# Kernel optimization log

Measured on AMD Instinct MI355X. Metric: run time of the kernel, lower is better.

## Reference

```python
import jax, jax.numpy as jnp
import numpy as np

_EPSILON = 1e-06
EPS = 0.05
MAX_ITER = 50
THRESHOLD = 0.001


def setup_inputs() -> dict:
    key = jax.random.key(0)
    k1, k2 = jax.random.split(key)
    source = jax.random.normal(k1, (8192, 64), dtype=jnp.float32)
    target = jax.random.normal(k2, (8192, 64), dtype=jnp.float32)
    return {"source": source, "target": target}


def _sinkhorn(source, target):
    source = source.astype(jnp.float32)
    target = target.astype(jnp.float32)
    # squared euclidean cost matrix [N, M] (cdist(p=2)**2)
    sq_s = jnp.sum(source * source, axis=1, keepdims=True)          # [N,1]
    sq_t = jnp.sum(target * target, axis=1, keepdims=True).T        # [1,M]
    cost = sq_s + sq_t - 2.0 * (source @ target.T)                  # [N,M]
    cost = jnp.maximum(cost, 0.0)

    n_source, n_target = cost.shape
    log_mu = jnp.full((n_source,), jnp.log(jnp.maximum(1.0 / n_source, _EPSILON)), dtype=jnp.float32)
    log_nu = jnp.full((n_target,), jnp.log(jnp.maximum(1.0 / n_target, _EPSILON)), dtype=jnp.float32)

    u0 = jnp.zeros((n_source,), dtype=jnp.float32)
    v0 = jnp.zeros((n_target,), dtype=jnp.float32)

    def step(carry, _):
        u, v, done = carry
        prev_u = u
        mc = (-cost + u[:, None] + v[None, :]) / EPS
        u_new = EPS * (log_mu - jax.nn.logsumexp(mc, axis=1)) + u
        mc2 = (-cost + u_new[:, None] + v[None, :]) / EPS
        v_new = EPS * (log_nu - jax.nn.logsumexp(mc2, axis=0)) + v
        # freeze state once converged (emulates the torch early break)
        u = jnp.where(done, u, u_new)
        v = jnp.where(done, v, v_new)
        done = done | (jnp.mean(jnp.abs(u_new - prev_u)) < THRESHOLD)
        return (u, v, done), None

    (u, v, _), _ = jax.lax.scan(step, (u0, v0, jnp.array(False)), None, length=MAX_ITER)

    transport_plan = jnp.exp((-cost + u[:, None] + v[None, :]) / EPS)
    return jnp.sum(transport_plan * cost)


def reference(source, target):
    return _sinkhorn(source, target)
```

## Files before the change

kernel.cpp:

```cpp
#include <hip/hip_runtime.h>

#define N      8192
#define KDIM   64
#define SCALE2     28.853900817779268f
#define INV_SCALE2 0.034657359027997264f
#define TWOSCALE   57.707801635558536f
#define EPSLN2     0.034657359027997264f
#define EPS_LOG_MU (-0.45054566736396444f)
#define THRESH     0.001f
#define NEG_BIG    (-1e30f)
#define NCHUNK  32
#define COLSPAN 256
#define NCT     16
#define ROWS_PER_BLOCK 128

typedef __attribute__((ext_vector_type(8))) short bf16x8;
typedef __attribute__((ext_vector_type(4))) float f32x4;

static __device__ __forceinline__ float exp2fast(float x) { return __builtin_amdgcn_exp2f(x); }
static __device__ __forceinline__ float log2fast(float x) { return __builtin_amdgcn_logf(x); }

static __device__ __forceinline__ unsigned short f2bf(float f) {
    unsigned u = __float_as_uint(f);
    u += 0x7FFFu + ((u >> 16) & 1u);
    return (unsigned short)(u >> 16);
}
static __device__ __forceinline__ float bf2f(unsigned short h) {
    return __uint_as_float(((unsigned)h) << 16);
}

static __device__ __forceinline__ void load16_to_lds(const void* gptr, void* lptr) {
    __builtin_amdgcn_global_load_lds(
        (const __attribute__((address_space(1))) unsigned int*)gptr,
        (__attribute__((address_space(3))) unsigned int*)lptr,
        16, 0, 0);
}

static __device__ __forceinline__ void stage_tile(
        const unsigned short* __restrict__ CPhi, const unsigned short* __restrict__ CPlo,
        char* ldsbuf, int jb, int wave, int swz) {
    const char* gsrc = (const char*)(wave < 2 ? CPhi : CPlo);
    const char* g = gsrc + (size_t)jb * 128 + (size_t)((wave & 1) * 1024 + swz);
    char* l = ldsbuf + (wave & 1) * 1024 + (wave >> 1) * 2048;
    load16_to_lds(g, l);
}

static __device__ __forceinline__ void load_held(
        const unsigned short* __restrict__ RPhi, const unsigned short* __restrict__ RPlo,
        int rowbase, int lrow, int kgrp, bf16x8 (&bh)[2][2], bf16x8 (&bl)[2][2]) {
#pragma unroll
    for (int it = 0; it < 2; ++it)
#pragma unroll
        for (int ks = 0; ks < 2; ++ks) {
            int boff = (rowbase + it * 16 + lrow) * KDIM + ks * 32 + kgrp * 8;
            bh[it][ks] = *reinterpret_cast<const bf16x8*>(RPhi + boff);
            bl[it][ks] = *reinterpret_cast<const bf16x8*>(RPlo + boff);
            asm volatile("" : "+v"(bh[it][ks]));
            asm volatile("" : "+v"(bl[it][ks]));
        }
}

static __device__ __forceinline__ void lse_loop(
        const unsigned short* __restrict__ CPhi, const unsigned short* __restrict__ CPlo,
        char* ldsA, const float* lds_alpha,
        const bf16x8 (&bh)[2][2], const bf16x8 (&bl)[2][2],
        int jbase0, int wave, int lane, int swz, float (&m)[2], float (&s)[2]) {
    const int lrow = lane & 15, kgrp = lane >> 4;
    const int ro = lrow * 128;
    const int x0 = ((kgrp)     ^ (lrow & 7)) * 16;
    const int x1 = ((kgrp + 4) ^ (lrow & 7)) * 16;
    int jb = jbase0;
    int buf = 0;
    for (int ct = 0; ct < NCT; ++ct) {
        if (ct + 1 < NCT)
            stage_tile(CPhi, CPlo, ldsA + ((buf ^ 1) << 12), jb + 16, wave, swz);

        float4 av = *reinterpret_cast<const float4*>(lds_alpha + ct * 16 + kgrp * 4);
        const char* base = ldsA + (buf << 12);
        bf16x8 ah0 = *reinterpret_cast<const bf16x8*>(base + ro + x0);
        bf16x8 ah1 = *reinterpret_cast<const bf16x8*>(base + ro + x1);
        bf16x8 al0 = *reinterpret_cast<const bf16x8*>(base + 2048 + ro + x0);
        bf16x8 al1 = *reinterpret_cast<const bf16x8*>(base + 2048 + ro + x1);

        f32x4 acc0 = {0.0f, 0.0f, 0.0f, 0.0f};
        f32x4 acc1 = {0.0f, 0.0f, 0.0f, 0.0f};
        acc0 = __builtin_amdgcn_mfma_f32_16x16x32_bf16(ah0, bh[0][0], acc0, 0, 0, 0);
        acc1 = __builtin_amdgcn_mfma_f32_16x16x32_bf16(ah0, bh[1][0], acc1, 0, 0, 0);
        acc0 = __builtin_amdgcn_mfma_f32_16x16x32_bf16(ah1, bh[0][1], acc0, 0, 0, 0);
        acc1 = __builtin_amdgcn_mfma_f32_16x16x32_bf16(ah1, bh[1][1], acc1, 0, 0, 0);
        acc0 = __builtin_amdgcn_mfma_f32_16x16x32_bf16(al0, bh[0][0], acc0, 0, 0, 0);
        acc1 = __builtin_amdgcn_mfma_f32_16x16x32_bf16(al0, bh[1][0], acc1, 0, 0, 0);
        acc0 = __builtin_amdgcn_mfma_f32_16x16x32_bf16(al1, bh[0][1], acc0, 0, 0, 0);
        acc1 = __builtin_amdgcn_mfma_f32_16x16x32_bf16(al1, bh[1][1], acc1, 0, 0, 0);
        acc0 = __builtin_amdgcn_mfma_f32_16x16x32_bf16(ah0, bl[0][0], acc0, 0, 0, 0);
        acc1 = __builtin_amdgcn_mfma_f32_16x16x32_bf16(ah0, bl[1][0], acc1, 0, 0, 0);
        acc0 = __builtin_amdgcn_mfma_f32_16x16x32_bf16(ah1, bl[0][1], acc0, 0, 0, 0);
        acc1 = __builtin_amdgcn_mfma_f32_16x16x32_bf16(ah1, bl[1][1], acc1, 0, 0, 0);

#pragma unroll
        for (int it = 0; it < 2; ++it) {
            f32x4 a = (it == 0) ? acc0 : acc1;
            float L0 = fmaf(TWOSCALE, a[0], av.x);
            float L1 = fmaf(TWOSCALE, a[1], av.y);
            float L2 = fmaf(TWOSCALE, a[2], av.z);
            float L3 = fmaf(TWOSCALE, a[3], av.w);
            float mx = fmaxf(fmaxf(L0, L1), fmaxf(L2, L3));
            float mn = fmaxf(m[it], mx);
            float rs = exp2fast(m[it] - mn);
            float e  = (exp2fast(L0 - mn) + exp2fast(L1 - mn)) +
                       (exp2fast(L2 - mn) + exp2fast(L3 - mn));
            s[it] = fmaf(s[it], rs, e);
            m[it] = mn;
        }
        __syncthreads();
        buf ^= 1; jb += 16;
    }
}

static __device__ __forceinline__ void write_partials(
        float (&m)[2], float (&s)[2], float* __restrict__ pm, float* __restrict__ ps,
        const float* __restrict__ sqr2, int ck, int rowbase, int lane) {
    const int lrow = lane & 15, kgrp = lane >> 4;
#pragma unroll
    for (int off = 16; off < 64; off <<= 1) {
#pragma unroll
        for (int it = 0; it < 2; ++it) {
            float mo = __shfl_xor(m[it], off);
            float so = __shfl_xor(s[it], off);
            float mn = fmaxf(m[it], mo);
            s[it] = s[it] * exp2fast(m[it] - mn) + so * exp2fast(mo - mn);
            m[it] = mn;
        }
    }
    if (kgrp == 0) {
#pragma unroll
        for (int it = 0; it < 2; ++it) {
            int row = rowbase + it * 16 + lrow;
            pm[(size_t)ck * N + row] = m[it] - sqr2[row];
            ps[(size_t)ck * N + row] = s[it];
        }
    }
}

__global__ void norms_kernel(const float* __restrict__ S, const float* __restrict__ T,
                             float* __restrict__ sq_s2, float* __restrict__ sq_t2) {
    int t = blockIdx.x * blockDim.x + threadIdx.x;
    const float* p = (t < N) ? S : T;
    int r = t & (N - 1);
    const float4* row = reinterpret_cast<const float4*>(p + (size_t)r * KDIM);
    float acc = 0.0f;
#pragma unroll
    for (int q = 0; q < KDIM / 4; ++q) {
        float4 a = row[q];
        acc += a.x * a.x + a.y * a.y + a.z * a.z + a.w * a.w;
    }
    if (t < N) sq_s2[r] = acc * SCALE2; else sq_t2[r] = acc * SCALE2;
}

__global__ void init_kernel(float* u, float* v, float* alphaT,
                            const float* __restrict__ sq_t2, int* doneArr) {
    int t = blockIdx.x * blockDim.x + threadIdx.x;
    if (t < N) { u[t] = 0.0f; v[t] = 0.0f; alphaT[t] = -sq_t2[t]; }
    if (t == 0) { doneArr[0] = 0; doneArr[1] = 0; }
}

__global__ void split_kernel(const float* __restrict__ S, const float* __restrict__ T,
                             unsigned short* __restrict__ Shi, unsigned short* __restrict__ Slo,
                             unsigned short* __restrict__ Thi, unsigned short* __restrict__ Tlo) {
    int t = blockIdx.x * 256 + threadIdx.x;
    const int half = (N * KDIM) / 4;
    const float* src = (t < half) ? S : T;
    unsigned short* dhi = (t < half) ? Shi : Thi;
    unsigned short* dlo = (t < half) ? Slo : Tlo;
    int e = (t < half) ? t : t - half;
    float4 x = reinterpret_cast<const float4*>(src)[e];
    unsigned short h0 = f2bf(x.x), h1 = f2bf(x.y), h2 = f2bf(x.z), h3 = f2bf(x.w);
    ushort4 hv = make_ushort4(h0, h1, h2, h3);
    ushort4 lv = make_ushort4(f2bf(x.x - bf2f(h0)), f2bf(x.y - bf2f(h1)),
                              f2bf(x.z - bf2f(h2)), f2bf(x.w - bf2f(h3)));
    reinterpret_cast<ushort4*>(dhi)[e] = hv;
    reinterpret_cast<ushort4*>(dlo)[e] = lv;
}

__global__ __launch_bounds__(256, 6) void row_lse(
        const unsigned short* __restrict__ CPhi, const unsigned short* __restrict__ CPlo,
        const unsigned short* __restrict__ RPhi, const unsigned short* __restrict__ RPlo,
        const float* __restrict__ alphaG, const float* __restrict__ sqr2,
        float* __restrict__ pm, float* __restrict__ ps,
        const int* __restrict__ done) {
    if (*done) return;
    __shared__ __align__(16) char ldsA[2 * 4096];
    __shared__ __align__(16) float lds_alpha[COLSPAN];
    const int wave = threadIdx.x >> 6, lane = threadIdx.x & 63;
    const int lrow = lane & 15, kgrp = lane >> 4;
    const int ck = blockIdx.x & 31, rb = blockIdx.x >> 5;
    const int rowbase = rb * ROWS_PER_BLOCK + wave * 32;
    const int jbase0 = ck * COLSPAN;
    const int swz = (lane >> 3) * 128 + (((lane & 7) ^ ((lane >> 3) & 7)) << 4);

    stage_tile(CPhi, CPlo, ldsA, jbase0, wave, swz);
    lds_alpha[threadIdx.x] = alphaG[jbase0 + threadIdx.x];

    bf16x8 bh[2][2], bl[2][2];
    load_held(RPhi, RPlo, rowbase, lrow, kgrp, bh, bl);

    float m[2] = {NEG_BIG, NEG_BIG}, s[2] = {0.0f, 0.0f};
    __syncthreads();

    lse_loop(CPhi, CPlo, ldsA, lds_alpha, bh, bl, jbase0, wave, lane, swz, m, s);
    write_partials(m, s, pm, ps, sqr2, ck, rowbase, lane);
}

__global__ __launch_bounds__(256, 6) void col_lse(
        const unsigned short* __restrict__ CPhi, const unsigned short* __restrict__ CPlo,
        const unsigned short* __restrict__ RPhi, const unsigned short* __restrict__ RPlo,
        const float* __restrict__ pm_in, const float* __restrict__ ps_in,
        const float* __restrict__ sqs2,
        float* __restrict__ u,
        float* __restrict__ blockDiff,
        const float* __restrict__ sqr2,
        float* __restrict__ pm, float* __restrict__ ps,
        const int* __restrict__ done) {
    if (*done) return;
    __shared__ __align__(16) char ldsA[2 * 4096];
    __shared__ __align__(16) float lds_alpha[COLSPAN];
    __shared__ float wsum[4];
    const int wave = threadIdx.x >> 6, lane = threadIdx.x & 63;
    const int lrow = lane & 15, kgrp = lane >> 4;
    const int ck = blockIdx.x & 31, rb = blockIdx.x >> 5;
    const int rowbase = rb * ROWS_PER_BLOCK + wave * 32;
    const int jbase0 = ck * COLSPAN;
    const int swz = (lane >> 3) * 128 + (((lane & 7) ^ ((lane >> 3) & 7)) << 4);

    stage_tile(CPhi, CPlo, ldsA, jbase0, wave, swz);

    {
        int j = jbase0 + threadIdx.x;
        float mm = NEG_BIG, ss = 0.0f;
#pragma unroll
        for (int c = 0; c < NCHUNK; ++c) {
            float mc = pm_in[(size_t)c * N + j];
            float sc = ps_in[(size_t)c * N + j];
            float mn = fmaxf(mm, mc);
            ss = ss * exp2fast(mm - mn) + sc * exp2fast(mc - mn);
            mm = mn;
        }
        float unew = EPS_LOG_MU - EPSLN2 * (mm + log2fast(ss));
        lds_alpha[threadIdx.x] = fmaf(unew, SCALE2, -sqs2[j]);
        if (rb == 0) {
            float d = fabsf(unew - u[j]);
            u[j] = unew;
#pragma unroll
            for (int off = 32; off; off >>= 1) d += __shfl_xor(d, off);
            if (lane == 0) wsum[wave] = d;
        }
    }

    bf16x8 bh[2][2], bl[2][2];
    load_held(RPhi, RPlo, rowbase, lrow, kgrp, bh, bl);

    float m[2] = {NEG_BIG, NEG_BIG}, s[2] = {0.0f, 0.0f};
    __syncthreads();
    if (rb == 0 && threadIdx.x == 0)
        blockDiff[ck] = wsum[0] + wsum[1] + wsum[2] + wsum[3];

    lse_loop(CPhi, CPlo, ldsA, lds_alpha, bh, bl, jbase0, wave, lane, swz, m, s);
    write_partials(m, s, pm, ps, sqr2, ck, rowbase, lane);
}

__global__ __launch_bounds__(256) void v_reduce(const float* __restrict__ pm,
                                                const float* __restrict__ ps,
                                                float* __restrict__ v,
                                                float* __restrict__ alphaT,
                                                const float* __restrict__ sqt2,
                                                const float* __restrict__ blockDiff,
                                                const int* __restrict__ dcur,
                                                int* __restrict__ dnext) {
    if (*dcur) {
        if (blockIdx.x == 0 && threadIdx.x == 0) *dnext = 1;
        return;
    }
    int j = blockIdx.x * 256 + threadIdx.x;
    float m = NEG_BIG, s = 0.0f;
#pragma unroll
    for (int c = 0; c < NCHUNK; ++c) {
        float mc = pm[(size_t)c * N + j];
        float sc = ps[(size_t)c * N + j];
        float mn = fmaxf(m, mc);
        s = s * exp2fast(m - mn) + sc * exp2fast(mc - mn);
        m = mn;
    }
    float vnew = EPS_LOG_MU - EPSLN2 * (m + log2fast(s));
    v[j] = vnew;
    alphaT[j] = fmaf(vnew, SCALE2, -sqt2[j]);

    if (blockIdx.x == 0 && threadIdx.x < 64) {
        float sum = (threadIdx.x < 32) ? blockDiff[threadIdx.x] : 0.0f;
#pragma unroll
        for (int off = 32; off; off >>= 1) sum += __shfl_xor(sum, off);
        if (threadIdx.x == 0)
            *dnext = (sum * (1.0f / (float)N) < THRESH) ? 1 : 0;
    }
}

__global__ __launch_bounds__(256, 6) void plan_mfma(
        const unsigned short* __restrict__ CPhi, const unsigned short* __restrict__ CPlo,
        const unsigned short* __restrict__ RPhi, const unsigned short* __restrict__ RPlo,
        const float* __restrict__ u, const float* __restrict__ v,
        const float* __restrict__ sqr2, const float* __restrict__ sqc2,
        float* __restrict__ part) {
    __shared__ __align__(16) char ldsA[2 * 4096];
    __shared__ __align__(16) float lds_v2[COLSPAN];
    __shared__ __align__(16) float lds_sqc[COLSPAN];
    __shared__ float wsum[4];
    const int wave = threadIdx.x >> 6, lane = threadIdx.x & 63;
    const int lrow = lane & 15, kgrp = lane >> 4;
    const int ck = blockIdx.x & 31, rb = blockIdx.x >> 5;
    const int rowbase = rb * ROWS_PER_BLOCK + wave * 32;
    const int jbase0 = ck * COLSPAN;
    const int swz = (lane >> 3) * 128 + (((lane & 7) ^ ((lane >> 3) & 7)) << 4);

    stage_tile(CPhi, CPlo, ldsA, jbase0, wave, swz);
    lds_v2[threadIdx.x]  = v[jbase0 + threadIdx.x] * SCALE2;
    lds_sqc[threadIdx.x] = sqc2[jbase0 + threadIdx.x];

    bf16x8 bh[2][2], bl[2][2];
    load_held(RPhi, RPlo, rowbase, lrow, kgrp, bh, bl);

    float sqr_i[2], u2_i[2];
#pragma unroll
    for (int it = 0; it < 2; ++it) {
        int row = rowbase + it * 16 + lrow;
        sqr_i[it] = sqr2[row];
        u2_i[it]  = u[row] * SCALE2;
    }

    float lsum = 0.0f;
    __syncthreads();

    const int ro = lrow * 128;
    const int x0 = ((kgrp)     ^ (lrow & 7)) * 16;
    const int x1 = ((kgrp + 4) ^ (lrow & 7)) * 16;
    int jb = jbase0;
    int buf = 0;
    for (int ct = 0; ct < NCT; ++ct) {
        if (ct + 1 < NCT)
            stage_tile(CPhi, CPlo, ldsA + ((buf ^ 1) << 12), jb + 16, wave, swz);

        float4 v2 = *reinterpret_cast<const float4*>(lds_v2 + ct * 16 + kgrp * 4);
        float4 sc = *reinterpret_cast<const float4*>(lds_sqc + ct * 16 + kgrp * 4);
        const char* base = ldsA + (buf << 12);
        bf16x8 ah0 = *reinterpret_cast<const bf16x8*>(base + ro + x0);
        bf16x8 ah1 = *reinterpret_cast<const bf16x8*>(base + ro + x1);
        bf16x8 al0 = *reinterpret_cast<const bf16x8*>(base + 2048 + ro + x0);
        bf16x8 al1 = *reinterpret_cast<const bf16x8*>(base + 2048 + ro + x1);

        f32x4 acc0 = {0.0f, 0.0f, 0.0f, 0.0f};
        f32x4 acc1 = {0.0f, 0.0f, 0.0f, 0.0f};
        acc0 = __builtin_amdgcn_mfma_f32_16x16x32_bf16(ah0, bh[0][0], acc0, 0, 0, 0);
        acc1 = __builtin_amdgcn_mfma_f32_16x16x32_bf16(ah0, bh[1][0], acc1, 0, 0, 0);
        acc0 = __builtin_amdgcn_mfma_f32_16x16x32_bf16(ah1, bh[0][1], acc0, 0, 0, 0);
        acc1 = __builtin_amdgcn_mfma_f32_16x16x32_bf16(ah1, bh[1][1], acc1, 0, 0, 0);
        acc0 = __builtin_amdgcn_mfma_f32_16x16x32_bf16(al0, bh[0][0], acc0, 0, 0, 0);
        acc1 = __builtin_amdgcn_mfma_f32_16x16x32_bf16(al0, bh[1][0], acc1, 0, 0, 0);
        acc0 = __builtin_amdgcn_mfma_f32_16x16x32_bf16(al1, bh[0][1], acc0, 0, 0, 0);
        acc1 = __builtin_amdgcn_mfma_f32_16x16x32_bf16(al1, bh[1][1], acc1, 0, 0, 0);
        acc0 = __builtin_amdgcn_mfma_f32_16x16x32_bf16(ah0, bl[0][0], acc0, 0, 0, 0);
        acc1 = __builtin_amdgcn_mfma_f32_16x16x32_bf16(ah0, bl[1][0], acc1, 0, 0, 0);
        acc0 = __builtin_amdgcn_mfma_f32_16x16x32_bf16(ah1, bl[0][1], acc0, 0, 0, 0);
        acc1 = __builtin_amdgcn_mfma_f32_16x16x32_bf16(ah1, bl[1][1], acc1, 0, 0, 0);

        float vs[4] = {v2.x, v2.y, v2.z, v2.w};
        float ss[4] = {sc.x, sc.y, sc.z, sc.w};
#pragma unroll
        for (int it = 0; it < 2; ++it) {
#pragma unroll
            for (int r = 0; r < 4; ++r) {
                float d = (it == 0) ? acc0[r] : acc1[r];
                float c2 = fmaxf(sqr_i[it] + ss[r] - TWOSCALE * d, 0.0f);
                lsum = fmaf(exp2fast(u2_i[it] + vs[r] - c2), c2, lsum);
            }
        }
        __syncthreads();
        buf ^= 1; jb += 16;
    }
    lsum *= INV_SCALE2;

#pragma unroll
    for (int off = 32; off; off >>= 1) lsum += __shfl_xor(lsum, off);
    if (lane == 0) wsum[wave] = lsum;
    __syncthreads();
    if (threadIdx.x == 0)
        part[blockIdx.x] = wsum[0] + wsum[1] + wsum[2] + wsum[3];
}

__global__ void final_reduce(const float* __restrict__ part, float* __restrict__ out) {
    int t = threadIdx.x;
    float sum = 0.0f;
    for (int i = t; i < 2048; i += 256) sum += part[i];
#pragma unroll
    for (int off = 32; off; off >>= 1) sum += __shfl_xor(sum, off);
    __shared__ float wsum[4];
    int lane = t & 63, wave = t >> 6;
    if (lane == 0) wsum[wave] = sum;
    __syncthreads();
    if (t == 0) out[0] = wsum[0] + wsum[1] + wsum[2] + wsum[3];
}

extern "C" void kernel_launch(void* const* d_in, const int* in_sizes, int n_in,
                              void* d_out, int out_size, void* d_ws, size_t ws_size,
                              hipStream_t stream) {
    const float* S = (const float*)d_in[0];
    const float* T = (const float*)d_in[1];
    float* out = (float*)d_out;

    unsigned short* us = (unsigned short*)d_ws;
    unsigned short* Shi = us;
    unsigned short* Slo = us + (size_t)N * KDIM;
    unsigned short* Thi = us + (size_t)2 * N * KDIM;
    unsigned short* Tlo = us + (size_t)3 * N * KDIM;
    float* w = (float*)(us + (size_t)4 * N * KDIM);
    size_t off = 0;
    float* sq_s2     = w + off; off += N;
    float* sq_t2     = w + off; off += N;
    float* u         = w + off; off += N;
    float* v         = w + off; off += N;
    float* alphaT    = w + off; off += N;
    float* pmA       = w + off; off += (size_t)NCHUNK * N;
    float* psA       = w + off; off += (size_t)NCHUNK * N;
    float* pmB       = w + off; off += (size_t)NCHUNK * N;
    float* psB       = w + off; off += (size_t)NCHUNK * N;
    float* blockDiff = w + off; off += 64;
    float* part      = w + off; off += 2048;
    int*   doneArr   = (int*)(w + off);

    hipLaunchKernelGGL(norms_kernel, dim3(64),   dim3(256), 0, stream, S, T, sq_s2, sq_t2);
    hipLaunchKernelGGL(init_kernel,  dim3(32),   dim3(256), 0, stream, u, v, alphaT, sq_t2, doneArr);
    hipLaunchKernelGGL(split_kernel, dim3(1024), dim3(256), 0, stream, S, T, Shi, Slo, Thi, Tlo);

    const int LSE_BLOCKS = (N / ROWS_PER_BLOCK) * NCHUNK;
    for (int it = 0; it < 50; ++it) {
        int* dcur  = doneArr + (it & 1);
        int* dnext = doneArr + ((it + 1) & 1);
        hipLaunchKernelGGL(row_lse, dim3(LSE_BLOCKS), dim3(256), 0, stream,
                           Thi, Tlo, Shi, Slo, alphaT, sq_s2, pmA, psA, dcur);
        hipLaunchKernelGGL(col_lse, dim3(LSE_BLOCKS), dim3(256), 0, stream,
                           Shi, Slo, Thi, Tlo, pmA, psA, sq_s2, u, blockDiff,
                           sq_t2, pmB, psB, dcur);
        hipLaunchKernelGGL(v_reduce, dim3(32), dim3(256), 0, stream,
                           pmB, psB, v, alphaT, sq_t2, blockDiff, dcur, dnext);
    }

    hipLaunchKernelGGL(plan_mfma, dim3(LSE_BLOCKS), dim3(256), 0, stream,
                       Thi, Tlo, Shi, Slo, u, v, sq_s2, sq_t2, part);
    hipLaunchKernelGGL(final_reduce, dim3(1), dim3(256), 0, stream, part, out);
}
```

Before: 3.665 ms.

## Triple-buffer column tiles with one barrier per iteration and partial vmcnt waits

Replaces the double-buffered LDS staging loop with a three-buffer ring, prefetching two tiles ahead. Each iteration now waits on all but the newest global load (vmcnt(1)) and issues a single barrier, instead of a full __syncthreads at the end of every iteration, and the loop is fully unrolled. The goal is to hide global-to-LDS latency and cut barrier stalls in the row, column and final LSE kernels. The cost is 50% more LDS per block, which may lower occupancy, and correctness now rests on the hand-written waitcnt counts matching the loads stage_tile actually issues.

```diff
diff --git a/kernel.cpp b/kernel.cpp
--- a/kernel.cpp
+++ b/kernel.cpp
@@ -60,6 +60,21 @@
         }
 }
 
+static __device__ __forceinline__ void barrier_lds_only() {
+    asm volatile("s_waitcnt lgkmcnt(0)" ::: "memory");
+    __builtin_amdgcn_sched_barrier(0);
+    __builtin_amdgcn_s_barrier();
+    __builtin_amdgcn_sched_barrier(0);
+}
+
+static __device__ __forceinline__ void pipe_wait(bool last) {
+    if (last) asm volatile("s_waitcnt vmcnt(0)" ::: "memory");
+    else      asm volatile("s_waitcnt vmcnt(1)" ::: "memory");
+    __builtin_amdgcn_sched_barrier(0);
+    __builtin_amdgcn_s_barrier();
+    __builtin_amdgcn_sched_barrier(0);
+}
+
 static __device__ __forceinline__ void lse_loop(
         const unsigned short* __restrict__ CPhi, const unsigned short* __restrict__ CPlo,
         char* ldsA, const float* lds_alpha,
@@ -69,14 +84,15 @@
     const int ro = lrow * 128;
     const int x0 = ((kgrp)     ^ (lrow & 7)) * 16;
     const int x1 = ((kgrp + 4) ^ (lrow & 7)) * 16;
-    int jb = jbase0;
-    int buf = 0;
+#pragma unroll
     for (int ct = 0; ct < NCT; ++ct) {
-        if (ct + 1 < NCT)
-            stage_tile(CPhi, CPlo, ldsA + ((buf ^ 1) << 12), jb + 16, wave, swz);
+        pipe_wait(ct == NCT - 1);
+        if (ct + 2 < NCT)
+            stage_tile(CPhi, CPlo, ldsA + ((ct + 2) % 3) * 4096,
+                       jbase0 + (ct + 2) * 16, wave, swz);
 
         float4 av = *reinterpret_cast<const float4*>(lds_alpha + ct * 16 + kgrp * 4);
-        const char* base = ldsA + (buf << 12);
+        const char* base = ldsA + (ct % 3) * 4096;
         bf16x8 ah0 = *reinterpret_cast<const bf16x8*>(base + ro + x0);
         bf16x8 ah1 = *reinterpret_cast<const bf16x8*>(base + ro + x1);
         bf16x8 al0 = *reinterpret_cast<const bf16x8*>(base + 2048 + ro + x0);
@@ -112,8 +128,6 @@
             s[it] = fmaf(s[it], rs, e);
             m[it] = mn;
         }
-        __syncthreads();
-        buf ^= 1; jb += 16;
     }
 }
 
@@ -189,7 +203,7 @@
         float* __restrict__ pm, float* __restrict__ ps,
         const int* __restrict__ done) {
     if (*done) return;
-    __shared__ __align__(16) char ldsA[2 * 4096];
+    __shared__ __align__(16) char ldsA[3 * 4096];
     __shared__ __align__(16) float lds_alpha[COLSPAN];
     const int wave = threadIdx.x >> 6, lane = threadIdx.x & 63;
     const int lrow = lane & 15, kgrp = lane >> 4;
@@ -198,14 +212,15 @@
     const int jbase0 = ck * COLSPAN;
     const int swz = (lane >> 3) * 128 + (((lane & 7) ^ ((lane >> 3) & 7)) << 4);
 
-    stage_tile(CPhi, CPlo, ldsA, jbase0, wave, swz);
+    stage_tile(CPhi, CPlo, ldsA,        jbase0,      wave, swz);
+    stage_tile(CPhi, CPlo, ldsA + 4096, jbase0 + 16, wave, swz);
     lds_alpha[threadIdx.x] = alphaG[jbase0 + threadIdx.x];
 
     bf16x8 bh[2][2], bl[2][2];
     load_held(RPhi, RPlo, rowbase, lrow, kgrp, bh, bl);
 
     float m[2] = {NEG_BIG, NEG_BIG}, s[2] = {0.0f, 0.0f};
-    __syncthreads();
+    barrier_lds_only();
 
     lse_loop(CPhi, CPlo, ldsA, lds_alpha, bh, bl, jbase0, wave, lane, swz, m, s);
     write_partials(m, s, pm, ps, sqr2, ck, rowbase, lane);
@@ -222,7 +237,7 @@
         float* __restrict__ pm, float* __restrict__ ps,
         const int* __restrict__ done) {
     if (*done) return;
-    __shared__ __align__(16) char ldsA[2 * 4096];
+    __shared__ __align__(16) char ldsA[3 * 4096];
     __shared__ __align__(16) float lds_alpha[COLSPAN];
     __shared__ float wsum[4];
     const int wave = threadIdx.x >> 6, lane = threadIdx.x & 63;
@@ -232,7 +247,8 @@
     const int jbase0 = ck * COLSPAN;
     const int swz = (lane >> 3) * 128 + (((lane & 7) ^ ((lane >> 3) & 7)) << 4);
 
-    stage_tile(CPhi, CPlo, ldsA, jbase0, wave, swz);
+    stage_tile(CPhi, CPlo, ldsA,        jbase0,      wave, swz);
+    stage_tile(CPhi, CPlo, ldsA + 4096, jbase0 + 16, wave, swz);
 
     {
         int j = jbase0 + threadIdx.x;
@@ -260,7 +276,7 @@
     load_held(RPhi, RPlo, rowbase, lrow, kgrp, bh, bl);
 
     float m[2] = {NEG_BIG, NEG_BIG}, s[2] = {0.0f, 0.0f};
-    __syncthreads();
+    barrier_lds_only();
     if (rb == 0 && threadIdx.x == 0)
         blockDiff[ck] = wsum[0] + wsum[1] + wsum[2] + wsum[3];
 
@@ -309,7 +325,7 @@
         const float* __restrict__ u, const float* __restrict__ v,
         const float* __restrict__ sqr2, const float* __restrict__ sqc2,
         float* __restrict__ part) {
-    __shared__ __align__(16) char ldsA[2 * 4096];
+    __shared__ __align__(16) char ldsA[3 * 4096];
     __shared__ __align__(16) float lds_v2[COLSPAN];
     __shared__ __align__(16) float lds_sqc[COLSPAN];
     __shared__ float wsum[4];
@@ -320,7 +336,8 @@
     const int jbase0 = ck * COLSPAN;
     const int swz = (lane >> 3) * 128 + (((lane & 7) ^ ((lane >> 3) & 7)) << 4);
 
-    stage_tile(CPhi, CPlo, ldsA, jbase0, wave, swz);
+    stage_tile(CPhi, CPlo, ldsA,        jbase0,      wave, swz);
+    stage_tile(CPhi, CPlo, ldsA + 4096, jbase0 + 16, wave, swz);
     lds_v2[threadIdx.x]  = v[jbase0 + threadIdx.x] * SCALE2;
     lds_sqc[threadIdx.x] = sqc2[jbase0 + threadIdx.x];
 
@@ -336,20 +353,21 @@
     }
 
     float lsum = 0.0f;
-    __syncthreads();
+    barrier_lds_only();
 
     const int ro = lrow * 128;
     const int x0 = ((kgrp)     ^ (lrow & 7)) * 16;
     const int x1 = ((kgrp + 4) ^ (lrow & 7)) * 16;
-    int jb = jbase0;
-    int buf = 0;
+#pragma unroll
     for (int ct = 0; ct < NCT; ++ct) {
-        if (ct + 1 < NCT)
-            stage_tile(CPhi, CPlo, ldsA + ((buf ^ 1) << 12), jb + 16, wave, swz);
+        pipe_wait(ct == NCT - 1);
+        if (ct + 2 < NCT)
+            stage_tile(CPhi, CPlo, ldsA + ((ct + 2) % 3) * 4096,
+                       jbase0 + (ct + 2) * 16, wave, swz);
 
         float4 v2 = *reinterpret_cast<const float4*>(lds_v2 + ct * 16 + kgrp * 4);
         float4 sc = *reinterpret_cast<const float4*>(lds_sqc + ct * 16 + kgrp * 4);
-        const char* base = ldsA + (buf << 12);
+        const char* base = ldsA + (ct % 3) * 4096;
         bf16x8 ah0 = *reinterpret_cast<const bf16x8*>(base + ro + x0);
         bf16x8 ah1 = *reinterpret_cast<const bf16x8*>(base + ro + x1);
         bf16x8 al0 = *reinterpret_cast<const bf16x8*>(base + 2048 + ro + x0);
@@ -381,8 +399,6 @@
                 lsum = fmaf(exp2fast(u2_i[it] + vs[r] - c2), c2, lsum);
             }
         }
-        __syncthreads();
-        buf ^= 1; jb += 16;
     }
     lsum *= INV_SCALE2;
 
```

Result: faster. 3.418 ms (-6.8%).
